# Kernel tuning notes

Measured on AMD Instinct MI355X. Metric: run time of the kernel, lower is better.

The kernel has to match this reference:

```python
import jax, jax.numpy as jnp
import numpy as np

N, E, NREL = 50000, 800000, 4
IN, EMB, HID, OUT, LVL = 32, 32, 32, 32, 3


def setup_inputs() -> dict:
    key = jax.random.key(0)
    ks = jax.random.split(key, 24)
    f32 = jnp.float32
    inp = {
        'x': jax.random.normal(ks[0], (N, IN), f32),
        'node_feat': jax.random.normal(ks[1], (N, EMB), f32),
        'edge_feat': jax.random.normal(ks[2], (E, EMB), f32),
        'src': jax.random.randint(ks[3], (E,), 0, N, jnp.int32),
        'dst': jax.random.randint(ks[4], (E,), 0, N, jnp.int32),
        'eid': jax.random.randint(ks[5], (E,), 0, NREL, jnp.int32),
        # layer 1 (in_feat=IN)
        'Wr1': jax.random.normal(ks[6], (NREL, IN + 2 * EMB, HID), f32) * 0.1,
        'attn_w1': jax.random.normal(ks[7], (EMB + HID, 1), f32) * 0.1,
        'loop_w1': jax.random.normal(ks[8], (EMB, HID), f32) * 0.1,
        'h_bias1': jax.random.normal(ks[9], (HID,), f32) * 0.1,
        'amrm_W1': jax.random.normal(ks[10], (LVL, HID, HID), f32) * 0.1,
        'amrm_b1': jax.random.normal(ks[11], (LVL, HID), f32) * 0.1,
        'amrm_a1': jax.random.normal(ks[12], (HID, 1), f32) * 0.1,
        # layer 2 (in_feat=HID)
        'Wr2': jax.random.normal(ks[13], (NREL, HID + 2 * EMB, OUT), f32) * 0.1,
        'attn_w2': jax.random.normal(ks[14], (EMB + OUT, 1), f32) * 0.1,
        'loop_w2': jax.random.normal(ks[15], (EMB, OUT), f32) * 0.1,
        'h_bias2': jax.random.normal(ks[16], (OUT,), f32) * 0.1,
        'amrm_W2': jax.random.normal(ks[17], (LVL, OUT, OUT), f32) * 0.1,
        'amrm_b2': jax.random.normal(ks[18], (LVL, OUT), f32) * 0.1,
        'amrm_a2': jax.random.normal(ks[19], (OUT, 1), f32) * 0.1,
    }
    return inp


def _rp_layer(feat, node_feat, src, dst, eid, edge_feat,
              Wr, attn_w, loop_w, h_bias, amrm_W, amrm_b, amrm_a):
    n = node_feat.shape[0]
    ones_e = jnp.ones((src.shape[0],), feat.dtype)
    # symmetric-ish degree norm: feat scaled by out-degree^-1/2
    deg_out = jnp.clip(jax.ops.segment_sum(ones_e, src, num_segments=n), 1.0)
    feat = feat * (deg_out ** -0.5)[:, None]
    # per-edge gather + relation-typed linear (grouped GEMM over NREL types)
    xe = jnp.concatenate([feat[src], edge_feat, node_feat[dst]], axis=1)  # [E, in+2*emb]
    m = jnp.zeros((xe.shape[0], Wr.shape[2]), feat.dtype)
    for r in range(Wr.shape[0]):
        m = m + jnp.where((eid == r)[:, None], xe @ Wr[r], 0.0)
    # edge attention + segment softmax over incoming edges per dst node
    z = jax.nn.leaky_relu(jnp.concatenate([node_feat[dst], m], axis=1) @ attn_w)  # [E,1]
    zmax = jax.ops.segment_max(z, dst, num_segments=n)
    ez = jnp.exp(z - zmax[dst])
    a = ez / jax.ops.segment_sum(ez, dst, num_segments=n)[dst]
    # scatter-sum aggregation
    h = jax.ops.segment_sum(a * m, dst, num_segments=n)
    h = h + node_feat @ loop_w
    deg_in = jnp.clip(jax.ops.segment_sum(ones_e, dst, num_segments=n), 1.0)
    h = h * (deg_in ** -0.5)[:, None] + h_bias
    # adaptive multi-level relation module
    lv = jax.nn.relu(jnp.einsum('nh,lho->nlo', h, amrm_W) + amrm_b[None])  # [N,L,O]
    sc = jax.nn.softmax(jnp.einsum('nlo,o->nl', lv, amrm_a[:, 0]), axis=-1)  # [N,L]
    return jnp.einsum('nl,nlo->no', sc, lv)


def reference(x, node_feat, edge_feat, src, dst, eid,
              Wr1, attn_w1, loop_w1, h_bias1, amrm_W1, amrm_b1, amrm_a1,
              Wr2, attn_w2, loop_w2, h_bias2, amrm_W2, amrm_b2, amrm_a2):
    h = jax.nn.relu(_rp_layer(x, node_feat, src, dst, eid, edge_feat,
                              Wr1, attn_w1, loop_w1, h_bias1, amrm_W1, amrm_b1, amrm_a1))
    h = jax.nn.relu(_rp_layer(h, node_feat, src, dst, eid, edge_feat,
                              Wr2, attn_w2, loop_w2, h_bias2, amrm_W2, amrm_b2, amrm_a2))
    return h
```

## Files before the change

### kernel.cpp

```cpp
#include <hip/hip_runtime.h>

#define NN 50000
#define NE 800000

#define O_DEGIN   0
#define O_DEGOUT  50048
#define O_ROWPTR  100096
#define O_CURSOR  150208
#define O_EINFO   200256
#define O_FEATN   1800256
#define O_ZF      3400256
#define O_ZNRD    3600320
#define O_VV      3800384
#define O_EZ      3800832
#define O_NFT     4600832
#define O_WDENT   6200832
#define O_YACCT   6450880
#define O_H1      19250880


__global__ __launch_bounds__(256) void k_deg(const int* __restrict__ src,
                                             const int* __restrict__ dst,
                                             int* degin, int* degout) {
    int e = blockIdx.x * 256 + threadIdx.x;
    if (e < NE) {
        atomicAdd(&degin[dst[e]], 1);
        atomicAdd(&degout[src[e]], 1);
    }
}

__global__ __launch_bounds__(1024) void k_scan(const int* __restrict__ degin,
                                               int* rowptr, int* cursor) {
    __shared__ int swsum[16];
    __shared__ int stot;
    int t = threadIdx.x;
    int lane = t & 63, w = t >> 6;
    int carry = 0;
    for (int ch = 0; ch < 4; ch++) {
        int base = ch * 16384 + t * 16;
        int v[16];
        int s = 0;
#pragma unroll
        for (int j = 0; j < 16; j++) {
            v[j] = (base + j < NN) ? degin[base + j] : 0;
            s += v[j];
        }
        int incl = s;
#pragma unroll
        for (int off = 1; off < 64; off <<= 1) {
            int x = __shfl_up(incl, off, 64);
            if (lane >= off) incl += x;
        }
        if (lane == 63) swsum[w] = incl;
        __syncthreads();
        if (w == 0) {
            int y = (lane < 16) ? swsum[lane] : 0;
            int yi = y;
#pragma unroll
            for (int off = 1; off < 16; off <<= 1) {
                int x = __shfl_up(yi, off, 64);
                if (lane >= off) yi += x;
            }
            if (lane < 16) swsum[lane] = yi - y;
            if (lane == 15) stot = yi;
        }
        __syncthreads();
        int excl = carry + swsum[w] + (incl - s);
#pragma unroll
        for (int j = 0; j < 16; j++) {
            if (base + j < NN) { rowptr[base + j] = excl; cursor[base + j] = excl; }
            excl += v[j];
        }
        carry += stot;
        __syncthreads();
    }
    if (t == 0) rowptr[NN] = carry;
}

__global__ __launch_bounds__(256) void k_scatter(const int* __restrict__ src,
                                                 const int* __restrict__ dst,
                                                 const int* __restrict__ eid,
                                                 int* cursor, int2* einfo) {
    int e = blockIdx.x * 256 + threadIdx.x;
    if (e >= NE) return;
    int slot = atomicAdd(&cursor[dst[e]], 1);
    einfo[slot] = make_int2(src[e] | (eid[e] << 20), e);
}


__global__ __launch_bounds__(384) void k_prevec(const float* __restrict__ Wr,
                                                const float* __restrict__ attw,
                                                float* __restrict__ vvec) {
    int t = threadIdx.x;
    int r = (t >> 5) & 3, k = t & 31, part = t >> 7;
    int row = (part == 0) ? (32 + k) : (part == 1) ? k : (64 + k);
    const float* wrow = Wr + (size_t)r * 3072 + row * 32;
    float s = 0.f;
#pragma unroll
    for (int c = 0; c < 32; c++) s += wrow[c] * attw[32 + c];
    vvec[t] = s;
}

__global__ __launch_bounds__(128) void k_nodeproj(const float* __restrict__ feat,
                                                  const float* __restrict__ nfeat,
                                                  const float* __restrict__ attw,
                                                  const float* __restrict__ vvec,
                                                  const int* __restrict__ degout,
                                                  float* __restrict__ featn,
                                                  float* __restrict__ nfT,
                                                  float* __restrict__ zF,
                                                  float* __restrict__ znrd) {
    int n = blockIdx.x * 128 + threadIdx.x;
    if (n >= NN) return;
    int dg = degout[n];
    float sc0 = rsqrtf((float)(dg > 1 ? dg : 1));
    const float* fin = feat + (size_t)n * 32;
    const float* nin = nfeat + (size_t)n * 32;
    float fv[32], nv[32];
#pragma unroll
    for (int k = 0; k < 32; k += 4) {
        float4 f4 = *(const float4*)&fin[k];
        fv[k] = f4.x * sc0; fv[k + 1] = f4.y * sc0;
        fv[k + 2] = f4.z * sc0; fv[k + 3] = f4.w * sc0;
        float4 n4 = *(const float4*)&nin[k];
        nv[k] = n4.x; nv[k + 1] = n4.y; nv[k + 2] = n4.z; nv[k + 3] = n4.w;
    }
    float* fo = featn + (size_t)n * 32;
#pragma unroll
    for (int k = 0; k < 32; k += 4)
        *(float4*)&fo[k] = make_float4(fv[k], fv[k + 1], fv[k + 2], fv[k + 3]);
#pragma unroll
    for (int k = 0; k < 32; k++) nfT[(size_t)k * NN + n] = nv[k];
    float zn = 0.f;
#pragma unroll
    for (int k = 0; k < 32; k++) zn += nv[k] * attw[k];
#pragma unroll
    for (int r = 0; r < 4; r++) {
        float zf = 0.f, zd = 0.f;
        const float* vf = vvec + 128 + r * 32;
        const float* vd = vvec + 256 + r * 32;
#pragma unroll
        for (int k = 0; k < 32; k++) { zf += fv[k] * vf[k]; zd += nv[k] * vd[k]; }
        zF[r * NN + n] = zf;
        znrd[r * NN + n] = zn + zd;
    }
}

__global__ __launch_bounds__(256) void k_ez(const int* __restrict__ src,
                                            const int* __restrict__ dst,
                                            const int* __restrict__ eid,
                                            const float* __restrict__ efeat,
                                            const float* __restrict__ zF,
                                            const float* __restrict__ znrd,
                                            const float* __restrict__ vvec,
                                            float* __restrict__ ez) {
    int e = blockIdx.x * 256 + threadIdx.x;
    int s = src[e], d = dst[e], r = eid[e];
    const float* er = efeat + (size_t)e * 32;
    float d0 = 0.f, d1 = 0.f, d2 = 0.f, d3 = 0.f;
#pragma unroll
    for (int k = 0; k < 32; k += 4) {
        float4 f = *(const float4*)&er[k];
        d0 += f.x * vvec[k]       + f.y * vvec[k + 1]
            + f.z * vvec[k + 2]   + f.w * vvec[k + 3];
        d1 += f.x * vvec[32 + k]  + f.y * vvec[33 + k]
            + f.z * vvec[34 + k]  + f.w * vvec[35 + k];
        d2 += f.x * vvec[64 + k]  + f.y * vvec[65 + k]
            + f.z * vvec[66 + k]  + f.w * vvec[67 + k];
        d3 += f.x * vvec[96 + k]  + f.y * vvec[97 + k]
            + f.z * vvec[98 + k]  + f.w * vvec[99 + k];
    }
    float dot = (r == 0) ? d0 : (r == 1) ? d1 : (r == 2) ? d2 : d3;
    float z = znrd[r * NN + d] + zF[r * NN + s] + dot;
    z = z > 0.f ? z : 0.01f * z;
    ez[e] = __expf(z);
}

__global__ __launch_bounds__(512) void k_agg(const int* __restrict__ rowptr,
                                             const int2* __restrict__ einfo,
                                             const float* __restrict__ ez,
                                             const float* __restrict__ efeat,
                                             const float* __restrict__ featn,
                                             float* __restrict__ yaccT,
                                             float* __restrict__ wdenT) {
    __shared__ float sT[256 * 9];
    int tid = threadIdx.x;
    int lane = tid & 63;
    int wid = tid >> 6;
    int n0 = blockIdx.x * 8;
    int n = n0 + wid;
    int c = lane & 31;
    int p = lane >> 5;

    int rp0 = rowptr[n];
    int deg = rowptr[n + 1] - rp0;

    float yf0 = 0.f, yf1 = 0.f, yf2 = 0.f, yf3 = 0.f;
    float ye0 = 0.f, ye1 = 0.f, ye2 = 0.f, ye3 = 0.f;
    float w0 = 0.f, w1 = 0.f, w2 = 0.f, w3 = 0.f, den = 0.f;

    int2 meA = make_int2(0, 0), meB = make_int2(0, 0);
    float ezA = 0.f, efA = 0.f, fnA = 0.f;
    if (p < deg) {
        meA = einfo[rp0 + p];
        ezA = ez[meA.y];
        efA = efeat[(size_t)meA.y * 32 + c];
        fnA = featn[(size_t)(meA.x & 0xFFFFF) * 32 + c];
    }
    if (p + 2 < deg) meB = einfo[rp0 + p + 2];

    for (int t = p; t < deg; t += 2) {
        float ezB = 0.f, efB = 0.f, fnB = 0.f;
        int2 meC = make_int2(0, 0);
        if (t + 2 < deg) {
            ezB = ez[meB.y];
            efB = efeat[(size_t)meB.y * 32 + c];
            fnB = featn[(size_t)(meB.x & 0xFFFFF) * 32 + c];
        }
        if (t + 4 < deg) meC = einfo[rp0 + t + 4];
        int rb = meA.x >> 20;
        float e0 = (rb == 0) ? ezA : 0.f;
        float e1 = (rb == 1) ? ezA : 0.f;
        float e2 = (rb == 2) ? ezA : 0.f;
        float e3 = (rb == 3) ? ezA : 0.f;
        yf0 += e0 * fnA; yf1 += e1 * fnA; yf2 += e2 * fnA; yf3 += e3 * fnA;
        ye0 += e0 * efA; ye1 += e1 * efA; ye2 += e2 * efA; ye3 += e3 * efA;
        w0 += e0; w1 += e1; w2 += e2; w3 += e3;
        den += ezA;
        meA = meB; ezA = ezB; efA = efB; fnA = fnB; meB = meC;
    }

    yf0 += __shfl_xor(yf0, 32); yf1 += __shfl_xor(yf1, 32);
    yf2 += __shfl_xor(yf2, 32); yf3 += __shfl_xor(yf3, 32);
    ye0 += __shfl_xor(ye0, 32); ye1 += __shfl_xor(ye1, 32);
    ye2 += __shfl_xor(ye2, 32); ye3 += __shfl_xor(ye3, 32);
    w0 += __shfl_xor(w0, 32); w1 += __shfl_xor(w1, 32);
    w2 += __shfl_xor(w2, 32); w3 += __shfl_xor(w3, 32);
    den += __shfl_xor(den, 32);

    if (lane < 5) {
        float wv = (lane == 0) ? w0 : (lane == 1) ? w1 : (lane == 2) ? w2
                 : (lane == 3) ? w3 : den;
        wdenT[lane * NN + n] = wv;
    }

    {
        int kb = 128 * p + c;
        sT[(kb +  0) * 9 + wid] = p ? ye0 : yf0;
        sT[(kb + 32) * 9 + wid] = p ? ye1 : yf1;
        sT[(kb + 64) * 9 + wid] = p ? ye2 : yf2;
        sT[(kb + 96) * 9 + wid] = p ? ye3 : yf3;
    }
    __syncthreads();
    int k = tid >> 1, hf = tid & 1;
    float4 v = make_float4(sT[k * 9 + hf * 4 + 0], sT[k * 9 + hf * 4 + 1],
                           sT[k * 9 + hf * 4 + 2], sT[k * 9 + hf * 4 + 3]);
    *(float4*)&yaccT[(size_t)k * NN + n0 + hf * 4] = v;
}

__global__ __launch_bounds__(256) void k_post(const int* __restrict__ rowptr,
                                              const float* __restrict__ yaccT,
                                              const float* __restrict__ wdenT,
                                              const float* __restrict__ nfT,
                                              const float* __restrict__ Wr,
                                              const float* __restrict__ lw,
                                              const float* __restrict__ hbias,
                                              const float* __restrict__ aW,
                                              const float* __restrict__ ab,
                                              const float* __restrict__ aa,
                                              float* __restrict__ out) {
    int n = blockIdx.x * 256 + threadIdx.x;
    if (n >= NN) return;
    int deg = rowptr[n + 1] - rowptr[n];
    float den = wdenT[4 * NN + n];
    float invden = (deg > 0) ? 1.f / den : 0.f;

    float nv[32];
#pragma unroll
    for (int k = 0; k < 32; k++) nv[k] = nfT[(size_t)k * NN + n];

    float acc[32];
#pragma unroll
    for (int i = 0; i < 32; i++) acc[i] = 0.f;
#pragma unroll
    for (int r = 0; r < 4; r++) {
        const float* W = Wr + (size_t)r * 3072;
        float wr = wdenT[r * NN + n];
        const float* ufc = yaccT + (size_t)(r * 32) * NN + n;
        const float* uec = yaccT + (size_t)(128 + r * 32) * NN + n;
        for (int k4 = 0; k4 < 32; k4 += 4) {
            float a0 = ufc[(size_t)(k4 + 0) * NN], a1 = ufc[(size_t)(k4 + 1) * NN];
            float a2 = ufc[(size_t)(k4 + 2) * NN], a3 = ufc[(size_t)(k4 + 3) * NN];
            float b0 = uec[(size_t)(k4 + 0) * NN], b1 = uec[(size_t)(k4 + 1) * NN];
            float b2 = uec[(size_t)(k4 + 2) * NN], b3 = uec[(size_t)(k4 + 3) * NN];
            float g0 = wr * nv[k4],     g1 = wr * nv[k4 + 1];
            float g2 = wr * nv[k4 + 2], g3 = wr * nv[k4 + 3];
            const float* Wk = W + k4 * 32;
#pragma unroll
            for (int i = 0; i < 32; i++)
                acc[i] += a0 * Wk[i]        + a1 * Wk[32 + i]
                        + a2 * Wk[64 + i]   + a3 * Wk[96 + i]
                        + b0 * Wk[1024 + i] + b1 * Wk[1056 + i]
                        + b2 * Wk[1088 + i] + b3 * Wk[1120 + i]
                        + g0 * Wk[2048 + i] + g1 * Wk[2080 + i]
                        + g2 * Wk[2112 + i] + g3 * Wk[2144 + i];
        }
    }

    float hsc = rsqrtf((float)(deg > 1 ? deg : 1));
    float h[32];
#pragma unroll
    for (int i = 0; i < 32; i++) h[i] = acc[i] * invden;
    for (int k4 = 0; k4 < 32; k4 += 4) {
        const float* Lk = lw + k4 * 32;
#pragma unroll
        for (int i = 0; i < 32; i++)
            h[i] += nv[k4] * Lk[i] + nv[k4 + 1] * Lk[32 + i]
                  + nv[k4 + 2] * Lk[64 + i] + nv[k4 + 3] * Lk[96 + i];
    }
#pragma unroll
    for (int i = 0; i < 32; i++) h[i] = h[i] * hsc + hbias[i];

    float s[3];
#pragma unroll
    for (int l = 0; l < 3; l++) {
        const float* A = aW + (size_t)l * 1024;
#pragma unroll
        for (int i = 0; i < 32; i++) acc[i] = ab[l * 32 + i];
        for (int k4 = 0; k4 < 32; k4 += 4) {
            const float* Ak = A + k4 * 32;
#pragma unroll
            for (int i = 0; i < 32; i++)
                acc[i] += h[k4] * Ak[i] + h[k4 + 1] * Ak[32 + i]
                        + h[k4 + 2] * Ak[64 + i] + h[k4 + 3] * Ak[96 + i];
        }
        float sl = 0.f;
#pragma unroll
        for (int i = 0; i < 32; i++) {
            float lv = acc[i] > 0.f ? acc[i] : 0.f;
            sl += lv * aa[i];
        }
        s[l] = sl;
    }
    float mx = fmaxf(s[0], fmaxf(s[1], s[2]));
    float e0 = __expf(s[0] - mx), e1 = __expf(s[1] - mx), e2 = __expf(s[2] - mx);
    float inv = 1.f / (e0 + e1 + e2);
    float scl[3] = {e0 * inv, e1 * inv, e2 * inv};

    float outv[32];
#pragma unroll
    for (int i = 0; i < 32; i++) outv[i] = 0.f;
#pragma unroll
    for (int l = 0; l < 3; l++) {
        const float* A = aW + (size_t)l * 1024;
#pragma unroll
        for (int i = 0; i < 32; i++) acc[i] = ab[l * 32 + i];
        for (int k4 = 0; k4 < 32; k4 += 4) {
            const float* Ak = A + k4 * 32;
#pragma unroll
            for (int i = 0; i < 32; i++)
                acc[i] += h[k4] * Ak[i] + h[k4 + 1] * Ak[32 + i]
                        + h[k4 + 2] * Ak[64 + i] + h[k4 + 3] * Ak[96 + i];
        }
#pragma unroll
        for (int i = 0; i < 32; i++) {
            float lv = acc[i] > 0.f ? acc[i] : 0.f;
            outv[i] += scl[l] * lv;
        }
    }
    float* op = out + (size_t)n * 32;
#pragma unroll
    for (int i = 0; i < 32; i += 4)
        *(float4*)&op[i] = make_float4(fmaxf(outv[i], 0.f), fmaxf(outv[i + 1], 0.f),
                                       fmaxf(outv[i + 2], 0.f), fmaxf(outv[i + 3], 0.f));
}


static void launch_layer(const float* feat, const float* nf, const float* efeat,
                         const int* src, const int* dst, const int* eid,
                         const float* Wr, const float* attw, const float* lw,
                         const float* hb, const float* aW, const float* ab,
                         const float* aa, float* wsf, int* wsi, float* out,
                         hipStream_t stream) {
    k_prevec<<<1, 384, 0, stream>>>(Wr, attw, wsf + O_VV);
    k_nodeproj<<<391, 128, 0, stream>>>(feat, nf, attw, wsf + O_VV, wsi + O_DEGOUT,
                                        wsf + O_FEATN, wsf + O_NFT,
                                        wsf + O_ZF, wsf + O_ZNRD);
    k_ez<<<3125, 256, 0, stream>>>(src, dst, eid, efeat, wsf + O_ZF, wsf + O_ZNRD,
                                   wsf + O_VV, wsf + O_EZ);
    k_agg<<<6250, 512, 0, stream>>>(wsi + O_ROWPTR, (const int2*)(wsi + O_EINFO),
                                    wsf + O_EZ, efeat, wsf + O_FEATN,
                                    wsf + O_YACCT, wsf + O_WDENT);
    k_post<<<196, 256, 0, stream>>>(wsi + O_ROWPTR, wsf + O_YACCT, wsf + O_WDENT,
                                    wsf + O_NFT, Wr, lw, hb, aW, ab, aa, out);
}

extern "C" void kernel_launch(void* const* d_in, const int* in_sizes, int n_in,
                              void* d_out, int out_size, void* d_ws, size_t ws_size,
                              hipStream_t stream) {
    const float* x     = (const float*)d_in[0];
    const float* nfeat = (const float*)d_in[1];
    const float* efeat = (const float*)d_in[2];
    const int*   src   = (const int*)d_in[3];
    const int*   dst   = (const int*)d_in[4];
    const int*   eid   = (const int*)d_in[5];
    const float* Wr1   = (const float*)d_in[6];
    const float* attw1 = (const float*)d_in[7];
    const float* lw1   = (const float*)d_in[8];
    const float* hb1   = (const float*)d_in[9];
    const float* aW1   = (const float*)d_in[10];
    const float* ab1   = (const float*)d_in[11];
    const float* aa1   = (const float*)d_in[12];
    const float* Wr2   = (const float*)d_in[13];
    const float* attw2 = (const float*)d_in[14];
    const float* lw2   = (const float*)d_in[15];
    const float* hb2   = (const float*)d_in[16];
    const float* aW2   = (const float*)d_in[17];
    const float* ab2   = (const float*)d_in[18];
    const float* aa2   = (const float*)d_in[19];

    float* wsf = (float*)d_ws;
    int*   wsi = (int*)d_ws;
    float* out = (float*)d_out;

    hipMemsetAsync(d_ws, 0, (size_t)O_ROWPTR * 4, stream);

    k_deg<<<NE / 256, 256, 0, stream>>>(src, dst, wsi + O_DEGIN, wsi + O_DEGOUT);
    k_scan<<<1, 1024, 0, stream>>>(wsi + O_DEGIN, wsi + O_ROWPTR, wsi + O_CURSOR);
    k_scatter<<<NE / 256, 256, 0, stream>>>(src, dst, eid, wsi + O_CURSOR,
                                            (int2*)(wsi + O_EINFO));

    launch_layer(x, nfeat, efeat, src, dst, eid, Wr1, attw1, lw1, hb1, aW1, ab1, aa1,
                 wsf, wsi, wsf + O_H1, stream);
    launch_layer(wsf + O_H1, nfeat, efeat, src, dst, eid, Wr2, attw2, lw2, hb2,
                 aW2, ab2, aa2, wsf, wsi, out, stream);
}
```

Measured before the change: 761.2 us.

## Split post-aggregation kernel by relation to raise parallelism

```diff
diff --git a/kernel.cpp b/kernel.cpp
--- a/kernel.cpp
+++ b/kernel.cpp
@@ -17,6 +17,7 @@
 #define O_WDENT   6200832
 #define O_YACCT   6450880
 #define O_H1      19250880
+#define O_PACC    20850880
 
 
 __global__ __launch_bounds__(256) void k_deg(const int* __restrict__ src,
@@ -258,17 +259,59 @@
     *(float4*)&yaccT[(size_t)k * NN + n0 + hf * 4] = v;
 }
 
-__global__ __launch_bounds__(256) void k_post(const int* __restrict__ rowptr,
-                                              const float* __restrict__ yaccT,
-                                              const float* __restrict__ wdenT,
-                                              const float* __restrict__ nfT,
-                                              const float* __restrict__ Wr,
-                                              const float* __restrict__ lw,
-                                              const float* __restrict__ hbias,
-                                              const float* __restrict__ aW,
-                                              const float* __restrict__ ab,
-                                              const float* __restrict__ aa,
-                                              float* __restrict__ out) {
+__global__ __launch_bounds__(256) void k_postA(const float* __restrict__ yaccT,
+                                               const float* __restrict__ wdenT,
+                                               const float* __restrict__ nfT,
+                                               const float* __restrict__ Wr,
+                                               float* __restrict__ pacc) {
+    int n = blockIdx.x * 256 + threadIdx.x;
+    if (n >= NN) return;
+    int r = blockIdx.y;
+
+    float nv[32];
+#pragma unroll
+    for (int k = 0; k < 32; k++) nv[k] = nfT[(size_t)k * NN + n];
+    float wr = wdenT[r * NN + n];
+
+    const float* W = Wr + (size_t)r * 3072;
+    const float* ufc = yaccT + (size_t)(r * 32) * NN + n;
+    const float* uec = yaccT + (size_t)(128 + r * 32) * NN + n;
+
+    float acc[32];
+#pragma unroll
+    for (int i = 0; i < 32; i++) acc[i] = 0.f;
+    for (int k4 = 0; k4 < 32; k4 += 4) {
+        float a0 = ufc[(size_t)(k4 + 0) * NN], a1 = ufc[(size_t)(k4 + 1) * NN];
+        float a2 = ufc[(size_t)(k4 + 2) * NN], a3 = ufc[(size_t)(k4 + 3) * NN];
+        float b0 = uec[(size_t)(k4 + 0) * NN], b1 = uec[(size_t)(k4 + 1) * NN];
+        float b2 = uec[(size_t)(k4 + 2) * NN], b3 = uec[(size_t)(k4 + 3) * NN];
+        float g0 = wr * nv[k4],     g1 = wr * nv[k4 + 1];
+        float g2 = wr * nv[k4 + 2], g3 = wr * nv[k4 + 3];
+        const float* Wk = W + k4 * 32;
+#pragma unroll
+        for (int i = 0; i < 32; i++)
+            acc[i] += a0 * Wk[i]        + a1 * Wk[32 + i]
+                    + a2 * Wk[64 + i]   + a3 * Wk[96 + i]
+                    + b0 * Wk[1024 + i] + b1 * Wk[1056 + i]
+                    + b2 * Wk[1088 + i] + b3 * Wk[1120 + i]
+                    + g0 * Wk[2048 + i] + g1 * Wk[2080 + i]
+                    + g2 * Wk[2112 + i] + g3 * Wk[2144 + i];
+    }
+    float* po = pacc + (size_t)(r * 32) * NN + n;
+#pragma unroll
+    for (int i = 0; i < 32; i++) po[(size_t)i * NN] = acc[i];
+}
+
+__global__ __launch_bounds__(256) void k_postB(const int* __restrict__ rowptr,
+                                               const float* __restrict__ pacc,
+                                               const float* __restrict__ wdenT,
+                                               const float* __restrict__ nfT,
+                                               const float* __restrict__ lw,
+                                               const float* __restrict__ hbias,
+                                               const float* __restrict__ aW,
+                                               const float* __restrict__ ab,
+                                               const float* __restrict__ aa,
+                                               float* __restrict__ out) {
     int n = blockIdx.x * 256 + threadIdx.x;
     if (n >= NN) return;
     int deg = rowptr[n + 1] - rowptr[n];
@@ -279,38 +322,15 @@
 #pragma unroll
     for (int k = 0; k < 32; k++) nv[k] = nfT[(size_t)k * NN + n];
 
-    float acc[32];
-#pragma unroll
-    for (int i = 0; i < 32; i++) acc[i] = 0.f;
-#pragma unroll
-    for (int r = 0; r < 4; r++) {
-        const float* W = Wr + (size_t)r * 3072;
-        float wr = wdenT[r * NN + n];
-        const float* ufc = yaccT + (size_t)(r * 32) * NN + n;
-        const float* uec = yaccT + (size_t)(128 + r * 32) * NN + n;
-        for (int k4 = 0; k4 < 32; k4 += 4) {
-            float a0 = ufc[(size_t)(k4 + 0) * NN], a1 = ufc[(size_t)(k4 + 1) * NN];
-            float a2 = ufc[(size_t)(k4 + 2) * NN], a3 = ufc[(size_t)(k4 + 3) * NN];
-            float b0 = uec[(size_t)(k4 + 0) * NN], b1 = uec[(size_t)(k4 + 1) * NN];
-            float b2 = uec[(size_t)(k4 + 2) * NN], b3 = uec[(size_t)(k4 + 3) * NN];
-            float g0 = wr * nv[k4],     g1 = wr * nv[k4 + 1];
-            float g2 = wr * nv[k4 + 2], g3 = wr * nv[k4 + 3];
-            const float* Wk = W + k4 * 32;
-#pragma unroll
-            for (int i = 0; i < 32; i++)
-                acc[i] += a0 * Wk[i]        + a1 * Wk[32 + i]
-                        + a2 * Wk[64 + i]   + a3 * Wk[96 + i]
-                        + b0 * Wk[1024 + i] + b1 * Wk[1056 + i]
-                        + b2 * Wk[1088 + i] + b3 * Wk[1120 + i]
-                        + g0 * Wk[2048 + i] + g1 * Wk[2080 + i]
-                        + g2 * Wk[2112 + i] + g3 * Wk[2144 + i];
-        }
-    }
-
-    float hsc = rsqrtf((float)(deg > 1 ? deg : 1));
     float h[32];
 #pragma unroll
-    for (int i = 0; i < 32; i++) h[i] = acc[i] * invden;
+    for (int i = 0; i < 32; i++) {
+        float s = pacc[(size_t)i * NN + n]
+                + pacc[(size_t)(32 + i) * NN + n]
+                + pacc[(size_t)(64 + i) * NN + n]
+                + pacc[(size_t)(96 + i) * NN + n];
+        h[i] = s * invden;
+    }
     for (int k4 = 0; k4 < 32; k4 += 4) {
         const float* Lk = lw + k4 * 32;
 #pragma unroll
@@ -318,9 +338,11 @@
             h[i] += nv[k4] * Lk[i] + nv[k4 + 1] * Lk[32 + i]
                   + nv[k4 + 2] * Lk[64 + i] + nv[k4 + 3] * Lk[96 + i];
     }
+    float hsc = rsqrtf((float)(deg > 1 ? deg : 1));
 #pragma unroll
     for (int i = 0; i < 32; i++) h[i] = h[i] * hsc + hbias[i];
 
+    float acc[32];
     float s[3];
 #pragma unroll
     for (int l = 0; l < 3; l++) {
@@ -391,8 +413,10 @@
     k_agg<<<6250, 512, 0, stream>>>(wsi + O_ROWPTR, (const int2*)(wsi + O_EINFO),
                                     wsf + O_EZ, efeat, wsf + O_FEATN,
                                     wsf + O_YACCT, wsf + O_WDENT);
-    k_post<<<196, 256, 0, stream>>>(wsi + O_ROWPTR, wsf + O_YACCT, wsf + O_WDENT,
-                                    wsf + O_NFT, Wr, lw, hb, aW, ab, aa, out);
+    k_postA<<<dim3(196, 4), 256, 0, stream>>>(wsf + O_YACCT, wsf + O_WDENT,
+                                              wsf + O_NFT, Wr, wsf + O_PACC);
+    k_postB<<<196, 256, 0, stream>>>(wsi + O_ROWPTR, wsf + O_PACC, wsf + O_WDENT,
+                                     wsf + O_NFT, lw, hb, aW, ab, aa, out);
 }
 
 extern "C" void kernel_launch(void* const* d_in, const int* in_sizes, int n_in,
```

New measurement: 703.8 us. 1.08x faster.
